# Performance work log

Measured on AMD Instinct MI355X. Metric: run time of the kernel, lower is better.

The kernel has to match this reference:

```python
import jax, jax.numpy as jnp
import numpy as np

B, S, H = 4, 2048, 1024
E, K = 8, 2
I_R, I_S = 4 * H, 8 * H
CAP_FACTOR = 1.25
SCALE = 1.0


def setup_inputs() -> dict:
    key = jax.random.key(0)
    ks = jax.random.split(key, 9)
    std = 0.02
    return {
        "x": jax.random.normal(ks[0], (B, S, H), jnp.float32),
        "router_w": std * jax.random.normal(ks[1], (E, H), jnp.float32),  # torch Linear [out,in]
        "rg": std * jax.random.normal(ks[2], (E, H, I_R), jnp.float32),  # gate_proj (transposed)
        "ru": std * jax.random.normal(ks[3], (E, H, I_R), jnp.float32),  # up_proj
        "rd": std * jax.random.normal(ks[4], (E, I_R, H), jnp.float32),  # down_proj
        "sg": std * jax.random.normal(ks[5], (H, I_S), jnp.float32),
        "su": std * jax.random.normal(ks[6], (H, I_S), jnp.float32),
        "sd": std * jax.random.normal(ks[7], (I_S, H), jnp.float32),
    }


def reference(x, router_w, rg, ru, rd, sg, su, sd):
    b, s, h = x.shape
    T = b * s
    capacity = max(int(CAP_FACTOR * T / E), 1)  # static
    xf = x.reshape(T, h)

    # ---- router (RMS-normed input, no training bias) ----
    eps = jnp.finfo(x.dtype).eps
    xn = xf * jax.lax.rsqrt(jnp.mean(xf * xf, axis=-1, keepdims=True) + eps)
    logits = xn @ router_w.T                      # [T,E]
    probs = jax.nn.softmax(logits, axis=-1)
    topk_p, topk_i = jax.lax.top_k(probs, K)      # [T,K]
    rw = topk_p / jnp.sum(topk_p, axis=-1, keepdims=True)

    one_hot = jax.nn.one_hot(topk_i, E, dtype=x.dtype)          # [T,K,E]
    mask = one_hot.sum(1)                                        # [T,E] 0/1
    wdense = (one_hot * rw[..., None]).sum(1)                    # [T,E] combine weights

    # ---- capacity-limited dispatch (first `capacity` tokens by index) ----
    sel = mask.T.astype(bool)                                    # [E,T]
    order = jnp.argsort(~sel, axis=1, stable=True)               # selected-first, token order
    dispatch = order[:, :capacity]                               # [E,C]
    count = sel.sum(axis=1)                                      # [E]
    valid = (jnp.arange(capacity)[None, :] < count[:, None]).astype(x.dtype)  # [E,C]

    xg = xf[dispatch]                                            # [E,C,H]
    gate = jax.nn.silu(jnp.einsum('ech,ehi->eci', xg, rg))
    up = jnp.einsum('ech,ehi->eci', xg, ru)
    eout = jnp.einsum('eci,eih->ech', gate * up, rd)             # [E,C,H]

    w = jnp.take_along_axis(wdense.T, dispatch, axis=1)          # [E,C]
    contrib = eout * (w * valid)[..., None]
    routed = jnp.zeros_like(xf).at[dispatch.reshape(-1)].add(contrib.reshape(-1, h))

    # ---- shared expert (dense SwiGLU on all tokens) ----
    shared = (jax.nn.silu(x @ sg) * (x @ su)) @ sd               # [B,S,H]

    return shared + SCALE * routed.reshape(b, s, h)
```

## Files before the change

kernel.cpp:

```cpp
#include <hip/hip_runtime.h>
#include <hip/hip_bf16.h>

#define TTOK 8192
#define HDIM 1024
#define ENUM 8
#define CAP  1280
#define IRD  4096
#define ISH  8192

typedef __hip_bfloat16 bf16;
typedef __bf16 bf16x8 __attribute__((ext_vector_type(8)));
typedef float f32x4 __attribute__((ext_vector_type(4)));

#define AS1(p) ((const __attribute__((address_space(1))) void*)(p))
#define AS3(p) ((__attribute__((address_space(3))) void*)(p))

__global__ __launch_bounds__(256) void router_kernel(
    const float* __restrict__ x, const float* __restrict__ rtw,
    bf16* __restrict__ xb,
    int* __restrict__ e0a, int* __restrict__ e1a,
    float* __restrict__ w0a, float* __restrict__ w1a,
    int* __restrict__ s0a, int* __restrict__ s1a)
{
    __shared__ float row[HDIM];
    __shared__ float ssred[4];
    __shared__ float lgl[ENUM];
    const int t = blockIdx.x;
    const int tid = threadIdx.x;
    const int lane = tid & 63, wv = tid >> 6;
    const float* xr = x + (size_t)t * HDIM;
    bf16* xbr = xb + (size_t)t * HDIM;
    float ss = 0.f;
    for (int i = tid; i < HDIM; i += 256) {
        float v = xr[i];
        row[i] = v;
        ss += v * v;
        xbr[i] = __float2bfloat16(v);
    }
    #pragma unroll
    for (int o = 32; o > 0; o >>= 1) ss += __shfl_down(ss, o, 64);
    if (lane == 0) ssred[wv] = ss;
    __syncthreads();
    for (int ee = 0; ee < 2; ++ee) {
        const int e = wv * 2 + ee;
        const float* we = rtw + e * HDIM;
        float p = 0.f;
        for (int i = lane; i < HDIM; i += 64) p += row[i] * we[i];
        #pragma unroll
        for (int o = 32; o > 0; o >>= 1) p += __shfl_down(p, o, 64);
        if (lane == 0) lgl[e] = p;
    }
    __syncthreads();
    if (tid == 0) {
        float tot = ssred[0] + ssred[1] + ssred[2] + ssred[3];
        float rstd = rsqrtf(tot / (float)HDIM + 1.1920929e-07f);
        float l[ENUM];
        #pragma unroll
        for (int e = 0; e < ENUM; ++e) l[e] = lgl[e] * rstd;
        int b0 = 0;
        #pragma unroll
        for (int e = 1; e < ENUM; ++e) if (l[e] > l[b0]) b0 = e;
        int b1 = (b0 == 0) ? 1 : 0;
        #pragma unroll
        for (int e = 0; e < ENUM; ++e) if (e != b0 && l[e] > l[b1]) b1 = e;
        float w0 = 1.f / (1.f + expf(l[b1] - l[b0]));
        e0a[t] = b0; e1a[t] = b1;
        w0a[t] = w0; w1a[t] = 1.f - w0;
        s0a[t] = -1; s1a[t] = -1;
    }
}

__global__ __launch_bounds__(256) void dispatch_kernel(
    const int* __restrict__ e0a, const int* __restrict__ e1a,
    int* __restrict__ disp, int* __restrict__ s0a, int* __restrict__ s1a)
{
    const int e = blockIdx.x;
    const int tid = threadIdx.x;
    const int lane = tid & 63, wv = tid >> 6;
    __shared__ int wcnt[4];
    for (int i = tid; i < CAP; i += 256) disp[e * CAP + i] = 0;
    __syncthreads();
    int run = 0;
    for (int base = 0; base < TTOK; base += 256) {
        const int t = base + tid;
        const bool f0 = (e0a[t] == e);
        const bool f1 = (e1a[t] == e);
        const bool f = f0 || f1;
        unsigned long long m = __ballot(f);
        int posw = __popcll(m & ((1ULL << lane) - 1ULL));
        if (lane == 0) wcnt[wv] = __popcll(m);
        __syncthreads();
        int off = 0;
        #pragma unroll
        for (int w = 0; w < 4; ++w) if (w < wv) off += wcnt[w];
        const int tot = wcnt[0] + wcnt[1] + wcnt[2] + wcnt[3];
        if (f) {
            const int pos = run + off + posw;
            if (pos < CAP) {
                disp[e * CAP + pos] = t;
                if (f0) s0a[t] = pos; else s1a[t] = pos;
            }
        }
        run += tot;
        __syncthreads();
    }
}

__global__ __launch_bounds__(256) void gather_kernel(
    const int* __restrict__ disp, const bf16* __restrict__ xb, bf16* __restrict__ xg)
{
    const int r = blockIdx.x;
    const int t = disp[r];
    const uint2* s = (const uint2*)(xb + (size_t)t * HDIM);
    uint2* d = (uint2*)(xg + (size_t)r * HDIM);
    d[threadIdx.x] = s[threadIdx.x];
}

__global__ __launch_bounds__(256) void tcvt_kernel(
    const float* __restrict__ in, bf16* __restrict__ out, int R, int C)
{
    __shared__ float tile[32][33];
    const size_t boff = (size_t)blockIdx.z * R * C;
    const int c0 = blockIdx.x * 32, r0 = blockIdx.y * 32;
    const int tx = threadIdx.x & 31, ty = threadIdx.x >> 5;
    #pragma unroll
    for (int i = 0; i < 4; ++i)
        tile[ty + i * 8][tx] = in[boff + (size_t)(r0 + ty + i * 8) * C + c0 + tx];
    __syncthreads();
    #pragma unroll
    for (int i = 0; i < 4; ++i)
        out[boff + (size_t)(c0 + ty + i * 8) * R + r0 + tx] =
            __float2bfloat16(tile[tx][ty + i * 8]);
}

template <int EPI>
__global__ __launch_bounds__(256) void gemm_bt(
    const bf16* __restrict__ A, const bf16* __restrict__ B,
    void* __restrict__ Cv, const bf16* __restrict__ Gaux,
    int M, int N, int K, long long sA, long long sB, long long sC)
{
    __shared__ bf16 ldsA[128 * 32];
    __shared__ bf16 ldsB[128 * 32];
    const int z = blockIdx.z;
    const bf16* Ab = A + (long long)z * sA;
    const bf16* Bb = B + (long long)z * sB;
    const int tid = threadIdx.x;
    const int lane = tid & 63, wv = tid >> 6;
    const int m0 = blockIdx.y * 128, n0 = blockIdx.x * 128;
    const int wr = (wv >> 1) * 64, wc = (wv & 1) * 64;
    const int srow = lane >> 2;
    const int skk  = (lane & 3) * 8;
    const int fr = lane & 15, fk = (lane >> 4) * 8;

    f32x4 acc[4][4] = {};

    for (int k0 = 0; k0 < K; k0 += 32) {
        #pragma unroll
        for (int rr = 0; rr < 2; ++rr) {
            const int c = wv * 2 + rr;
            const int row = c * 16 + srow;
            const bf16* ga = Ab + (long long)(m0 + row) * K + (k0 + skk);
            const bf16* gb = Bb + (long long)(n0 + row) * K + (k0 + skk);
            __builtin_amdgcn_global_load_lds(AS1(ga), AS3(ldsA + c * 512), 16, 0, 0);
            __builtin_amdgcn_global_load_lds(AS1(gb), AS3(ldsB + c * 512), 16, 0, 0);
        }
        __syncthreads();
        bf16x8 af[4], bfr[4];
        #pragma unroll
        for (int i = 0; i < 4; ++i)
            af[i] = *(const bf16x8*)(ldsA + (wr + i * 16 + fr) * 32 + fk);
        #pragma unroll
        for (int j = 0; j < 4; ++j)
            bfr[j] = *(const bf16x8*)(ldsB + (wc + j * 16 + fr) * 32 + fk);
        #pragma unroll
        for (int i = 0; i < 4; ++i)
            #pragma unroll
            for (int j = 0; j < 4; ++j)
                acc[i][j] = __builtin_amdgcn_mfma_f32_16x16x32_bf16(
                    af[i], bfr[j], acc[i][j], 0, 0, 0);
        __syncthreads();
    }

    const int erow = wr + (lane >> 4) * 4;
    const int ecol = wc + (lane & 15);
    #pragma unroll
    for (int i = 0; i < 4; ++i) {
        #pragma unroll
        for (int j = 0; j < 4; ++j) {
            #pragma unroll
            for (int r = 0; r < 4; ++r) {
                const long long row = m0 + erow + i * 16 + r;
                const long long col = n0 + ecol + j * 16;
                const long long idx = (long long)z * sC + row * N + col;
                const float v = acc[i][j][r];
                if (EPI == 0) {
                    ((bf16*)Cv)[idx] = __float2bfloat16(v);
                } else if (EPI == 1) {
                    const float g = __bfloat162float(Gaux[idx]);
                    const float sg_ = g / (1.f + __expf(-g));
                    ((bf16*)Cv)[idx] = __float2bfloat16(sg_ * v);
                } else {
                    ((float*)Cv)[idx] = v;
                }
            }
        }
    }
}

template <int EPI>
__global__ __launch_bounds__(512, 2) void gemm256(
    const bf16* __restrict__ A, const bf16* __restrict__ B,
    void* __restrict__ Cv, const bf16* __restrict__ Gaux,
    int M, int N, int K, long long sA, long long sB, long long sC)
{
    __shared__ bf16 lds[2][2][16384];
    const int z = blockIdx.z;
    const bf16* Ab = A + (long long)z * sA;
    const bf16* Bb = B + (long long)z * sB;
    const int tid  = threadIdx.x;
    const int lane = tid & 63, wv = tid >> 6;
    const int wm = wv >> 2, wn = wv & 3;
    const int m0 = blockIdx.y * 256, n0 = blockIdx.x * 256;
    const int fr = lane & 15, fq = lane >> 4;

    const int srl  = (wv << 4) + (lane >> 2);
    const int sswz = ((srl >> 3) & 1) << 4;
    const int scol = ((lane & 3) << 3) ^ sswz;
    auto STAGE = [&](int d, int mx, int h, int kt) {
        const bf16* gb = (mx ? Bb : Ab);
        const int grow = (mx ? n0 : m0) + (h << 7) + srl;
        const bf16* g0 = gb + (long long)grow * K + (kt << 6) + scol;
        bf16* l0 = &lds[d][mx][(h << 13) + (wv << 9)];
        __builtin_amdgcn_global_load_lds(AS1(g0),      AS3(l0),        16, 0, 0);
        __builtin_amdgcn_global_load_lds(AS1(g0 + 32), AS3(l0 + 4096), 16, 0, 0);
    };
    auto LDA = [&](int d, int i, int ks) -> bf16x8 {
        const int row = i * 16 + fr;
        const int col = (fq << 3) ^ (((row >> 3) & 1) << 4);
        return *(const bf16x8*)&lds[d][0][(wm << 13) + (ks << 12) + row * 32 + col];
    };
    auto LDB = [&](int d, int j, int ks) -> bf16x8 {
        const int rr = wn * 64 + j * 16 + fr;
        const int h = rr >> 7, row = rr & 127;
        const int col = (fq << 3) ^ (((row >> 3) & 1) << 4);
        return *(const bf16x8*)&lds[d][1][(h << 13) + (ks << 12) + row * 32 + col];
    };

    f32x4 acc[8][4] = {};
    bf16x8 af[4][2], bfg[4][2];
    const int nkt = K >> 6;

    STAGE(0, 0, 0, 0); STAGE(0, 0, 1, 0); STAGE(0, 1, 0, 0); STAGE(0, 1, 1, 0);
    if (nkt > 1) {
        STAGE(1, 1, 0, 1); STAGE(1, 1, 1, 1);
        asm volatile("s_waitcnt vmcnt(4)" ::: "memory");
    } else {
        asm volatile("s_waitcnt vmcnt(0)" ::: "memory");
    }
    asm volatile("s_barrier" ::: "memory");

    for (int kt = 0; kt < nkt; ++kt) {
        const int d = kt & 1;
        #pragma unroll
        for (int i = 0; i < 4; ++i) { af[i][0] = LDA(d, i, 0); af[i][1] = LDA(d, i, 1); }
        #pragma unroll
        for (int j = 0; j < 2; ++j) { bfg[j][0] = LDB(d, j, 0); bfg[j][1] = LDB(d, j, 1); }
        if (kt + 1 < nkt) STAGE(d ^ 1, 0, 0, kt + 1);
        asm volatile("s_waitcnt lgkmcnt(8)" ::: "memory");
        asm volatile("s_barrier" ::: "memory");
        __builtin_amdgcn_s_setprio(1);
        #pragma unroll
        for (int i = 0; i < 4; ++i)
            #pragma unroll
            for (int j = 0; j < 2; ++j) {
                acc[i][j] = __builtin_amdgcn_mfma_f32_16x16x32_bf16(af[i][0], bfg[j][0], acc[i][j], 0, 0, 0);
                acc[i][j] = __builtin_amdgcn_mfma_f32_16x16x32_bf16(af[i][1], bfg[j][1], acc[i][j], 0, 0, 0);
            }
        __builtin_amdgcn_s_setprio(0);
        asm volatile("s_barrier" ::: "memory");
        #pragma unroll
        for (int j = 2; j < 4; ++j) { bfg[j][0] = LDB(d, j, 0); bfg[j][1] = LDB(d, j, 1); }
        if (kt + 1 < nkt) STAGE(d ^ 1, 0, 1, kt + 1);
        asm volatile("s_barrier" ::: "memory");
        __builtin_amdgcn_s_setprio(1);
        #pragma unroll
        for (int i = 0; i < 4; ++i)
            #pragma unroll
            for (int j = 2; j < 4; ++j) {
                acc[i][j] = __builtin_amdgcn_mfma_f32_16x16x32_bf16(af[i][0], bfg[j][0], acc[i][j], 0, 0, 0);
                acc[i][j] = __builtin_amdgcn_mfma_f32_16x16x32_bf16(af[i][1], bfg[j][1], acc[i][j], 0, 0, 0);
            }
        __builtin_amdgcn_s_setprio(0);
        asm volatile("s_barrier" ::: "memory");
        #pragma unroll
        for (int i = 0; i < 4; ++i) { af[i][0] = LDA(d, i + 4, 0); af[i][1] = LDA(d, i + 4, 1); }
        if (kt + 2 < nkt) STAGE(d, 1, 0, kt + 2);
        asm volatile("s_barrier" ::: "memory");
        __builtin_amdgcn_s_setprio(1);
        #pragma unroll
        for (int i = 0; i < 4; ++i)
            #pragma unroll
            for (int j = 0; j < 2; ++j) {
                acc[i + 4][j] = __builtin_amdgcn_mfma_f32_16x16x32_bf16(af[i][0], bfg[j][0], acc[i + 4][j], 0, 0, 0);
                acc[i + 4][j] = __builtin_amdgcn_mfma_f32_16x16x32_bf16(af[i][1], bfg[j][1], acc[i + 4][j], 0, 0, 0);
            }
        __builtin_amdgcn_s_setprio(0);
        asm volatile("s_barrier" ::: "memory");
        if (kt + 2 < nkt) STAGE(d, 1, 1, kt + 2);
        if (kt + 1 < nkt) {
            if (kt + 2 < nkt) { asm volatile("s_waitcnt vmcnt(4)" ::: "memory"); }
            else              { asm volatile("s_waitcnt vmcnt(0)" ::: "memory"); }
        }
        asm volatile("s_barrier" ::: "memory");
        __builtin_amdgcn_s_setprio(1);
        #pragma unroll
        for (int i = 0; i < 4; ++i)
            #pragma unroll
            for (int j = 2; j < 4; ++j) {
                acc[i + 4][j] = __builtin_amdgcn_mfma_f32_16x16x32_bf16(af[i][0], bfg[j][0], acc[i + 4][j], 0, 0, 0);
                acc[i + 4][j] = __builtin_amdgcn_mfma_f32_16x16x32_bf16(af[i][1], bfg[j][1], acc[i + 4][j], 0, 0, 0);
            }
        __builtin_amdgcn_s_setprio(0);
        asm volatile("s_barrier" ::: "memory");
    }

    const int erow0 = m0 + wm * 128 + fq * 4;
    const int ecol0 = n0 + wn * 64 + fr;
    #pragma unroll
    for (int i = 0; i < 8; ++i) {
        #pragma unroll
        for (int j = 0; j < 4; ++j) {
            #pragma unroll
            for (int r = 0; r < 4; ++r) {
                const long long row = erow0 + i * 16 + r;
                const long long col = ecol0 + j * 16;
                const long long idx = (long long)z * sC + row * N + col;
                const float v = acc[i][j][r];
                if (EPI == 0) {
                    ((bf16*)Cv)[idx] = __float2bfloat16(v);
                } else if (EPI == 1) {
                    const float g = __bfloat162float(Gaux[idx]);
                    const float sg_ = g / (1.f + __expf(-g));
                    ((bf16*)Cv)[idx] = __float2bfloat16(sg_ * v);
                } else {
                    ((float*)Cv)[idx] = v;
                }
            }
        }
    }
}

__global__ __launch_bounds__(256) void combine_kernel(
    float* __restrict__ out, const float* __restrict__ eout,
    const int* __restrict__ e0a, const int* __restrict__ e1a,
    const float* __restrict__ w0a, const float* __restrict__ w1a,
    const int* __restrict__ s0a, const int* __restrict__ s1a)
{
    const int t = blockIdx.x;
    const int tid = threadIdx.x;
    float4* op = (float4*)(out + (size_t)t * HDIM);
    float4 v = op[tid];
    const int s0 = s0a[t], s1 = s1a[t];
    if (s0 >= 0) {
        const float4* p = (const float4*)(eout + ((size_t)e0a[t] * CAP + s0) * HDIM);
        const float w = w0a[t];
        float4 c = p[tid];
        v.x += w * c.x; v.y += w * c.y; v.z += w * c.z; v.w += w * c.w;
    }
    if (s1 >= 0) {
        const float4* p = (const float4*)(eout + ((size_t)e1a[t] * CAP + s1) * HDIM);
        const float w = w1a[t];
        float4 c = p[tid];
        v.x += w * c.x; v.y += w * c.y; v.z += w * c.z; v.w += w * c.w;
    }
    op[tid] = v;
}

extern "C" void kernel_launch(void* const* d_in, const int* in_sizes, int n_in,
                              void* d_out, int out_size, void* d_ws, size_t ws_size,
                              hipStream_t stream)
{
    const float* x   = (const float*)d_in[0];
    const float* rtw = (const float*)d_in[1];
    const float* rg  = (const float*)d_in[2];
    const float* ru  = (const float*)d_in[3];
    const float* rd  = (const float*)d_in[4];
    const float* sg  = (const float*)d_in[5];
    const float* su  = (const float*)d_in[6];
    const float* sd  = (const float*)d_in[7];
    float* out = (float*)d_out;

    char* w = (char*)d_ws;
    auto alloc = [&](size_t n) { char* p = w; w += (n + 255) & ~(size_t)255; return p; };
    bf16*  xb   = (bf16*)alloc((size_t)TTOK * HDIM * 2);
    bf16*  xg   = (bf16*)alloc((size_t)ENUM * CAP * HDIM * 2);
    bf16*  gbuf = (bf16*)alloc((size_t)ENUM * CAP * IRD * 2);
    float* eout = (float*)alloc((size_t)ENUM * CAP * HDIM * 4);
    bf16*  wbuf = (bf16*)alloc((size_t)ENUM * HDIM * IRD * 2);
    bf16*  sgt  = (bf16*)alloc((size_t)HDIM * ISH * 2);
    bf16*  sut  = (bf16*)alloc((size_t)HDIM * ISH * 2);
    bf16*  sdt  = (bf16*)alloc((size_t)HDIM * ISH * 2);
    int*   e0a  = (int*)alloc(TTOK * 4);
    int*   e1a  = (int*)alloc(TTOK * 4);
    float* w0a  = (float*)alloc(TTOK * 4);
    float* w1a  = (float*)alloc(TTOK * 4);
    int*   s0a  = (int*)alloc(TTOK * 4);
    int*   s1a  = (int*)alloc(TTOK * 4);
    int*   disp = (int*)alloc(ENUM * CAP * 4);

    router_kernel<<<TTOK, 256, 0, stream>>>(x, rtw, xb, e0a, e1a, w0a, w1a, s0a, s1a);
    dispatch_kernel<<<ENUM, 256, 0, stream>>>(e0a, e1a, disp, s0a, s1a);
    gather_kernel<<<ENUM * CAP, 256, 0, stream>>>(disp, xb, xg);

    tcvt_kernel<<<dim3(IRD / 32, HDIM / 32, ENUM), 256, 0, stream>>>(rg, wbuf, HDIM, IRD);
    gemm256<0><<<dim3(IRD / 256, CAP / 256, ENUM), 512, 0, stream>>>(
        xg, wbuf, gbuf, nullptr, CAP, IRD, HDIM,
        (long long)CAP * HDIM, (long long)IRD * HDIM, (long long)CAP * IRD);
    tcvt_kernel<<<dim3(IRD / 32, HDIM / 32, ENUM), 256, 0, stream>>>(ru, wbuf, HDIM, IRD);
    gemm256<1><<<dim3(IRD / 256, CAP / 256, ENUM), 512, 0, stream>>>(
        xg, wbuf, gbuf, gbuf, CAP, IRD, HDIM,
        (long long)CAP * HDIM, (long long)IRD * HDIM, (long long)CAP * IRD);
    tcvt_kernel<<<dim3(HDIM / 32, IRD / 32, ENUM), 256, 0, stream>>>(rd, wbuf, IRD, HDIM);
    gemm_bt<2><<<dim3(HDIM / 128, CAP / 128, ENUM), 256, 0, stream>>>(
        gbuf, wbuf, eout, nullptr, CAP, HDIM, IRD,
        (long long)CAP * IRD, (long long)HDIM * IRD, (long long)CAP * HDIM);

    tcvt_kernel<<<dim3(ISH / 32, HDIM / 32, 1), 256, 0, stream>>>(sg, sgt, HDIM, ISH);
    tcvt_kernel<<<dim3(ISH / 32, HDIM / 32, 1), 256, 0, stream>>>(su, sut, HDIM, ISH);
    tcvt_kernel<<<dim3(HDIM / 32, ISH / 32, 1), 256, 0, stream>>>(sd, sdt, ISH, HDIM);
    for (int c = 0; c < 2; ++c) {
        const bf16* Ax = xb + (size_t)c * 4096 * HDIM;
        gemm256<0><<<dim3(ISH / 256, 4096 / 256, 1), 512, 0, stream>>>(
            Ax, sgt, gbuf, nullptr, 4096, ISH, HDIM, 0, 0, 0);
        gemm256<1><<<dim3(ISH / 256, 4096 / 256, 1), 512, 0, stream>>>(
            Ax, sut, gbuf, gbuf, 4096, ISH, HDIM, 0, 0, 0);
        gemm_bt<2><<<dim3(HDIM / 128, 4096 / 128, 1), 256, 0, stream>>>(
            gbuf, sdt, out + (size_t)c * 4096 * HDIM, nullptr, 4096, HDIM, ISH, 0, 0, 0);
    }
    combine_kernel<<<TTOK, 256, 0, stream>>>(out, eout, e0a, e1a, w0a, w1a, s0a, s1a);
}
```

Measured before the change: 1.606 ms.

## Split shared expert along intermediate dim and use 256-tile GEMM for down projections

Removes the 128x128 gemm_bt kernel and runs every down projection on the larger 256x256 gemm256 kernel, adding an accumulate epilogue (EPI 3). The shared expert is now split along the intermediate dimension into two halves over all 8192 tokens instead of two token halves. The second down-projection half accumulates into the fp32 output. The sd transpose is done per half so that each chunk of the transposed weight is contiguous. The aim is higher MFMA efficiency from larger tiles. The cost is an extra read-modify-write of the fp32 output, and the down GEMMs with N=1024 now launch fewer blocks (4 column tiles), which may lower occupancy.

New measurement: 1.438 ms. 1.12x faster.

```diff
diff --git a/kernel.cpp b/kernel.cpp
--- a/kernel.cpp
+++ b/kernel.cpp
@@ -131,80 +131,6 @@
     for (int i = 0; i < 4; ++i)
         out[boff + (size_t)(c0 + ty + i * 8) * R + r0 + tx] =
             __float2bfloat16(tile[tx][ty + i * 8]);
-}
-
-template <int EPI>
-__global__ __launch_bounds__(256) void gemm_bt(
-    const bf16* __restrict__ A, const bf16* __restrict__ B,
-    void* __restrict__ Cv, const bf16* __restrict__ Gaux,
-    int M, int N, int K, long long sA, long long sB, long long sC)
-{
-    __shared__ bf16 ldsA[128 * 32];
-    __shared__ bf16 ldsB[128 * 32];
-    const int z = blockIdx.z;
-    const bf16* Ab = A + (long long)z * sA;
-    const bf16* Bb = B + (long long)z * sB;
-    const int tid = threadIdx.x;
-    const int lane = tid & 63, wv = tid >> 6;
-    const int m0 = blockIdx.y * 128, n0 = blockIdx.x * 128;
-    const int wr = (wv >> 1) * 64, wc = (wv & 1) * 64;
-    const int srow = lane >> 2;
-    const int skk  = (lane & 3) * 8;
-    const int fr = lane & 15, fk = (lane >> 4) * 8;
-
-    f32x4 acc[4][4] = {};
-
-    for (int k0 = 0; k0 < K; k0 += 32) {
-        #pragma unroll
-        for (int rr = 0; rr < 2; ++rr) {
-            const int c = wv * 2 + rr;
-            const int row = c * 16 + srow;
-            const bf16* ga = Ab + (long long)(m0 + row) * K + (k0 + skk);
-            const bf16* gb = Bb + (long long)(n0 + row) * K + (k0 + skk);
-            __builtin_amdgcn_global_load_lds(AS1(ga), AS3(ldsA + c * 512), 16, 0, 0);
-            __builtin_amdgcn_global_load_lds(AS1(gb), AS3(ldsB + c * 512), 16, 0, 0);
-        }
-        __syncthreads();
-        bf16x8 af[4], bfr[4];
-        #pragma unroll
-        for (int i = 0; i < 4; ++i)
-            af[i] = *(const bf16x8*)(ldsA + (wr + i * 16 + fr) * 32 + fk);
-        #pragma unroll
-        for (int j = 0; j < 4; ++j)
-            bfr[j] = *(const bf16x8*)(ldsB + (wc + j * 16 + fr) * 32 + fk);
-        #pragma unroll
-        for (int i = 0; i < 4; ++i)
-            #pragma unroll
-            for (int j = 0; j < 4; ++j)
-                acc[i][j] = __builtin_amdgcn_mfma_f32_16x16x32_bf16(
-                    af[i], bfr[j], acc[i][j], 0, 0, 0);
-        __syncthreads();
-    }
-
-    const int erow = wr + (lane >> 4) * 4;
-    const int ecol = wc + (lane & 15);
-    #pragma unroll
-    for (int i = 0; i < 4; ++i) {
-        #pragma unroll
-        for (int j = 0; j < 4; ++j) {
-            #pragma unroll
-            for (int r = 0; r < 4; ++r) {
-                const long long row = m0 + erow + i * 16 + r;
-                const long long col = n0 + ecol + j * 16;
-                const long long idx = (long long)z * sC + row * N + col;
-                const float v = acc[i][j][r];
-                if (EPI == 0) {
-                    ((bf16*)Cv)[idx] = __float2bfloat16(v);
-                } else if (EPI == 1) {
-                    const float g = __bfloat162float(Gaux[idx]);
-                    const float sg_ = g / (1.f + __expf(-g));
-                    ((bf16*)Cv)[idx] = __float2bfloat16(sg_ * v);
-                } else {
-                    ((float*)Cv)[idx] = v;
-                }
-            }
-        }
-    }
 }
 
 template <int EPI>
@@ -342,8 +268,10 @@
                     const float g = __bfloat162float(Gaux[idx]);
                     const float sg_ = g / (1.f + __expf(-g));
                     ((bf16*)Cv)[idx] = __float2bfloat16(sg_ * v);
+                } else if (EPI == 2) {
+                    ((float*)Cv)[idx] = v;
                 } else {
-                    ((float*)Cv)[idx] = v;
+                    ((float*)Cv)[idx] += v;
                 }
             }
         }
@@ -421,21 +349,29 @@
         xg, wbuf, gbuf, gbuf, CAP, IRD, HDIM,
         (long long)CAP * HDIM, (long long)IRD * HDIM, (long long)CAP * IRD);
     tcvt_kernel<<<dim3(HDIM / 32, IRD / 32, ENUM), 256, 0, stream>>>(rd, wbuf, IRD, HDIM);
-    gemm_bt<2><<<dim3(HDIM / 128, CAP / 128, ENUM), 256, 0, stream>>>(
+    gemm256<2><<<dim3(HDIM / 256, CAP / 256, ENUM), 512, 0, stream>>>(
         gbuf, wbuf, eout, nullptr, CAP, HDIM, IRD,
         (long long)CAP * IRD, (long long)HDIM * IRD, (long long)CAP * HDIM);
 
     tcvt_kernel<<<dim3(ISH / 32, HDIM / 32, 1), 256, 0, stream>>>(sg, sgt, HDIM, ISH);
     tcvt_kernel<<<dim3(ISH / 32, HDIM / 32, 1), 256, 0, stream>>>(su, sut, HDIM, ISH);
-    tcvt_kernel<<<dim3(HDIM / 32, ISH / 32, 1), 256, 0, stream>>>(sd, sdt, ISH, HDIM);
+    for (int c = 0; c < 2; ++c)
+        tcvt_kernel<<<dim3(HDIM / 32, 4096 / 32, 1), 256, 0, stream>>>(
+            sd + (size_t)c * 4096 * HDIM, sdt + (size_t)c * HDIM * 4096, 4096, HDIM);
     for (int c = 0; c < 2; ++c) {
-        const bf16* Ax = xb + (size_t)c * 4096 * HDIM;
-        gemm256<0><<<dim3(ISH / 256, 4096 / 256, 1), 512, 0, stream>>>(
-            Ax, sgt, gbuf, nullptr, 4096, ISH, HDIM, 0, 0, 0);
-        gemm256<1><<<dim3(ISH / 256, 4096 / 256, 1), 512, 0, stream>>>(
-            Ax, sut, gbuf, gbuf, 4096, ISH, HDIM, 0, 0, 0);
-        gemm_bt<2><<<dim3(HDIM / 128, 4096 / 128, 1), 256, 0, stream>>>(
-            gbuf, sdt, out + (size_t)c * 4096 * HDIM, nullptr, 4096, HDIM, ISH, 0, 0, 0);
+        const bf16* Bg = sgt + (size_t)c * 4096 * HDIM;
+        const bf16* Bu = sut + (size_t)c * 4096 * HDIM;
+        const bf16* Bd = sdt + (size_t)c * HDIM * 4096;
+        gemm256<0><<<dim3(4096 / 256, TTOK / 256, 1), 512, 0, stream>>>(
+            xb, Bg, gbuf, nullptr, TTOK, 4096, HDIM, 0, 0, 0);
+        gemm256<1><<<dim3(4096 / 256, TTOK / 256, 1), 512, 0, stream>>>(
+            xb, Bu, gbuf, gbuf, TTOK, 4096, HDIM, 0, 0, 0);
+        if (c == 0)
+            gemm256<2><<<dim3(HDIM / 256, TTOK / 256, 1), 512, 0, stream>>>(
+                gbuf, Bd, out, nullptr, TTOK, HDIM, 4096, 0, 0, 0);
+        else
+            gemm256<3><<<dim3(HDIM / 256, TTOK / 256, 1), 512, 0, stream>>>(
+                gbuf, Bd, out, nullptr, TTOK, HDIM, 4096, 0, 0, 0);
     }
     combine_kernel<<<TTOK, 256, 0, stream>>>(out, eout, e0a, e1a, w0a, w1a, s0a, s1a);
 }
```
